# Performance work log

Hardware: AMD Instinct MI355X
Metric: run time of the kernel (lower is better)

The kernel has to match this reference:

```python
import jax, jax.numpy as jnp
import numpy as np

B, T, D = 32, 1024, 1024
PCA_DIM = 256
NS = 4
NC = 1024
SEC = PCA_DIM // NS


def setup_inputs() -> dict:
    key = jax.random.key(0)
    k1, k2, k3 = jax.random.split(key, 3)
    inputs = jax.random.normal(k1, (B, T, D), dtype=jnp.float32)
    # variance_scaling(1.0, 'fan_avg', 'normal'): std = sqrt(2 / (fan_in + fan_out))
    pca_proj = jax.random.normal(k2, (D, PCA_DIM), dtype=jnp.float32) * np.float32(np.sqrt(2.0 / (D + PCA_DIM)))
    pre_bias = jnp.zeros((1, D), dtype=jnp.float32)
    # per-section codebooks, variance_scaling(0.1, 'fan_avg', 'normal')
    codebooks = jax.random.normal(k3, (NS, NC, SEC), dtype=jnp.float32) * np.float32(np.sqrt(0.1 * 2.0 / (NC + SEC)))
    return {"inputs": inputs, "pca_proj": pca_proj, "pre_bias": pre_bias, "codebooks": codebooks}


def reference(inputs, pca_proj, pre_bias, codebooks):
    in_shape = inputs.shape
    d = in_shape[-1]
    flat = inputs.reshape(-1, d)  # [N, D]
    n = flat.shape[0]
    # --- PCA projection + reconstruction / decorrelation losses ---
    projected = (flat + pre_bias) @ pca_proj            # [N, P]
    unprojected = projected @ pca_proj.T - pre_bias     # [N, D]
    l2_loss = jnp.mean(jnp.sqrt(jnp.sum(jnp.square(flat - unprojected), axis=-1)))
    cov = projected.T @ projected / n                   # [P, P]
    cov_loss = jnp.mean(jnp.square(cov - jnp.eye(pca_proj.shape[1], dtype=projected.dtype)))
    pca_loss = l2_loss + cov_loss
    # --- per-section vector quantization ---
    ns, nc, sec = codebooks.shape
    secs = projected.reshape(n, ns, sec).transpose(1, 0, 2)  # [ns, N, sec] == jnp.split along -1

    def quantize_section(x, cb):
        # x: [N, sec], cb: [nc, sec]; squared-L2 cdist via expansion
        dist = (jnp.sum(x * x, axis=1, keepdims=True)
                - 2.0 * (x @ cb.T)
                + jnp.sum(cb * cb, axis=1)[None, :])    # [N, nc]
        idx = jnp.argmin(dist, axis=1)                  # [N]
        q = cb[idx]                                     # gather == one_hot @ cb
        loss = jnp.square(q - jax.lax.stop_gradient(x))  # [N, sec]
        q_st = x + jax.lax.stop_gradient(q - x)         # straight-through
        return q_st, loss, idx

    q, sec_loss, idx = jax.vmap(quantize_section)(secs, codebooks)  # [ns,N,sec] x2, [ns,N]
    quantized = q.transpose(1, 0, 2).reshape(n, ns * sec)           # concat sections -> [N, P]
    quantized = (quantized @ pca_proj.T - pre_bias).reshape(in_shape)  # pca_unproject
    nn_idx = idx.reshape((ns,) + in_shape[:-1])                     # [ns, B, T]
    quantization_loss = jnp.mean(sec_loss.reshape((ns,) + in_shape[:-1] + (sec,)), axis=0) + pca_loss
    codebook = jax.lax.stop_gradient(codebooks.reshape(ns * nc, sec))
    cluster_counts = jnp.ones((ns, nc), dtype=jnp.float32)  # eval mode: jnp.ones init, no EMA
    return quantized, quantization_loss, nn_idx, codebook, cluster_counts
```

## Files before the change

kernel.cpp:

```cpp
#include <hip/hip_runtime.h>
#include <math.h>

#define NROW 32768
#define DIM  1024
#define PDIM 256
#define NSEC 4
#define NCODE 1024
#define SECD 64

__global__ __launch_bounds__(256, 4) void k_proj(const float* __restrict__ X,
                                                 const float* __restrict__ W,
                                                 const float* __restrict__ bias,
                                                 float* __restrict__ p0) {
    __shared__ __align__(16) float As[16][68];
    __shared__ __align__(16) float Bs[16][256];
    const int t  = threadIdx.x;
    const int ry = t >> 5;
    const int rx = t & 31;
    const int rb = blockIdx.x * 64;
    const int z  = blockIdx.z;
    const int k0 = z * 384;
    const int kn = (z == 2) ? 256 : 384;
    const int lr = t >> 2;
    const int ks = (t & 3) * 4;
    const int wv = t >> 6;
    const int ln = t & 63;
    const int gsw = ((ln & 31) << 1) | (ln >> 5);
    float* outp = p0 + (size_t)z * ((size_t)NROW * PDIM);
    float acc[8][8] = {};
    for (int kc = k0; kc < k0 + kn; kc += 16) {
        #pragma unroll
        for (int j = 0; j < 4; ++j) {
            const int krow = wv * 4 + j;
            __builtin_amdgcn_global_load_lds(
                (const __attribute__((address_space(1))) void*)(W + (size_t)(kc + krow) * PDIM + gsw * 4),
                (__attribute__((address_space(3))) void*)(&Bs[krow][0]),
                16, 0, 0);
        }
        float4 a = *(const float4*)&X[(size_t)(rb + lr) * DIM + kc + ks];
        float4 c = *(const float4*)&bias[kc + ks];
        As[ks + 0][lr] = a.x + c.x;
        As[ks + 1][lr] = a.y + c.y;
        As[ks + 2][lr] = a.z + c.z;
        As[ks + 3][lr] = a.w + c.w;
        __syncthreads();
        #pragma unroll
        for (int k = 0; k < 16; ++k) {
            float4 x0 = *(const float4*)&As[k][ry * 8];
            float4 x1 = *(const float4*)&As[k][ry * 8 + 4];
            float4 y0 = *(const float4*)&Bs[k][rx * 4];
            float4 y1 = *(const float4*)&Bs[k][128 + rx * 4];
            float aa[8] = {x0.x, x0.y, x0.z, x0.w, x1.x, x1.y, x1.z, x1.w};
            float bb[8] = {y0.x, y0.y, y0.z, y0.w, y1.x, y1.y, y1.z, y1.w};
            #pragma unroll
            for (int i = 0; i < 8; ++i)
                #pragma unroll
                for (int j = 0; j < 8; ++j)
                    acc[i][j] = fmaf(aa[i], bb[j], acc[i][j]);
        }
        __syncthreads();
    }
    #pragma unroll
    for (int i = 0; i < 8; ++i) {
        const size_t base = (size_t)(rb + ry * 8 + i) * PDIM + rx * 8;
        *(float4*)&outp[base]     = make_float4(acc[i][0], acc[i][1], acc[i][2], acc[i][3]);
        *(float4*)&outp[base + 4] = make_float4(acc[i][4], acc[i][5], acc[i][6], acc[i][7]);
    }
}

__global__ __launch_bounds__(256) void k_comb(float* __restrict__ p) {
    const size_t i = ((size_t)blockIdx.x * 256 + threadIdx.x) * 4;
    float4 a = *(const float4*)&p[i];
    float4 b = *(const float4*)&p[i + 8388608];
    float4 c = *(const float4*)&p[i + 16777216];
    float4 r;
    r.x = __fadd_rn(__fadd_rn(a.x, b.x), c.x);
    r.y = __fadd_rn(__fadd_rn(a.y, b.y), c.y);
    r.z = __fadd_rn(__fadd_rn(a.z, b.z), c.z);
    r.w = __fadd_rn(__fadd_rn(a.w, b.w), c.w);
    *(float4*)&p[i] = r;
}

__global__ __launch_bounds__(256, 4) void k_pm(const float* __restrict__ P,
                                               const float* __restrict__ M,
                                               float* __restrict__ PMa,
                                               float* __restrict__ PMb) {
    __shared__ __align__(16) float As[16][68];
    __shared__ __align__(16) float Bs[16][256];
    const int t  = threadIdx.x;
    const int ry = t >> 5;
    const int rx = t & 31;
    const int rb = blockIdx.x * 64;
    const int z  = blockIdx.z;
    const int k0 = z * 128;
    const int lr = t >> 2;
    const int ks = (t & 3) * 4;
    const int wv = t >> 6;
    const int ln = t & 63;
    const int gsw = ((ln & 31) << 1) | (ln >> 5);
    float* outp = z ? PMb : PMa;
    float acc[8][8] = {};
    for (int kc = k0; kc < k0 + 128; kc += 16) {
        #pragma unroll
        for (int j = 0; j < 4; ++j) {
            const int krow = wv * 4 + j;
            __builtin_amdgcn_global_load_lds(
                (const __attribute__((address_space(1))) void*)(M + (size_t)(kc + krow) * PDIM + gsw * 4),
                (__attribute__((address_space(3))) void*)(&Bs[krow][0]),
                16, 0, 0);
        }
        float4 a = *(const float4*)&P[(size_t)(rb + lr) * PDIM + kc + ks];
        As[ks + 0][lr] = a.x;
        As[ks + 1][lr] = a.y;
        As[ks + 2][lr] = a.z;
        As[ks + 3][lr] = a.w;
        __syncthreads();
        #pragma unroll
        for (int k = 0; k < 16; ++k) {
            float4 x0 = *(const float4*)&As[k][ry * 8];
            float4 x1 = *(const float4*)&As[k][ry * 8 + 4];
            float4 y0 = *(const float4*)&Bs[k][rx * 4];
            float4 y1 = *(const float4*)&Bs[k][128 + rx * 4];
            float aa[8] = {x0.x, x0.y, x0.z, x0.w, x1.x, x1.y, x1.z, x1.w};
            float bb[8] = {y0.x, y0.y, y0.z, y0.w, y1.x, y1.y, y1.z, y1.w};
            #pragma unroll
            for (int i = 0; i < 8; ++i)
                #pragma unroll
                for (int j = 0; j < 8; ++j)
                    acc[i][j] = fmaf(aa[i], bb[j], acc[i][j]);
        }
        __syncthreads();
    }
    #pragma unroll
    for (int i = 0; i < 8; ++i) {
        const size_t base = (size_t)(rb + ry * 8 + i) * PDIM + rx * 8;
        *(float4*)&outp[base]     = make_float4(acc[i][0], acc[i][1], acc[i][2], acc[i][3]);
        *(float4*)&outp[base + 4] = make_float4(acc[i][4], acc[i][5], acc[i][6], acc[i][7]);
    }
}

__global__ __launch_bounds__(256) void k_wtw(const float* __restrict__ W,
                                             float* __restrict__ M) {
    __shared__ float As[16][64];
    __shared__ float Bs[16][64];
    const int t = threadIdx.x;
    const int tx = t & 15, ty = t >> 4;
    const int ib = blockIdx.x * 64;
    const int jb = blockIdx.y * 64;
    const int sk = t >> 4;
    const int sc = (t & 15) * 4;
    float acc[4][4] = {};
    for (int kc = 0; kc < DIM; kc += 16) {
        float4 a = *(const float4*)&W[(size_t)(kc + sk) * PDIM + ib + sc];
        float4 b = *(const float4*)&W[(size_t)(kc + sk) * PDIM + jb + sc];
        *(float4*)&As[sk][sc] = a;
        *(float4*)&Bs[sk][sc] = b;
        __syncthreads();
        #pragma unroll
        for (int k = 0; k < 16; ++k) {
            float4 a4 = *(const float4*)&As[k][ty * 4];
            float4 b4 = *(const float4*)&Bs[k][tx * 4];
            float aa[4] = {a4.x, a4.y, a4.z, a4.w};
            float bb[4] = {b4.x, b4.y, b4.z, b4.w};
            #pragma unroll
            for (int i = 0; i < 4; ++i)
                #pragma unroll
                for (int j = 0; j < 4; ++j)
                    acc[i][j] = fmaf(aa[i], bb[j], acc[i][j]);
        }
        __syncthreads();
    }
    #pragma unroll
    for (int i = 0; i < 4; ++i)
        #pragma unroll
        for (int j = 0; j < 4; ++j)
            M[(size_t)(ib + ty * 4 + i) * PDIM + jb + tx * 4 + j] = acc[i][j];
}

__global__ __launch_bounds__(256) void k_xn2(const float* __restrict__ X,
                                             const float* __restrict__ bias,
                                             float* __restrict__ xn2) {
    const int n = blockIdx.x * 4 + (threadIdx.x >> 6);
    const int lane = threadIdx.x & 63;
    float s = 0.0f;
    #pragma unroll
    for (int i = 0; i < 4; ++i) {
        float4 x = *(const float4*)&X[(size_t)n * DIM + i * 256 + lane * 4];
        float4 b = *(const float4*)&bias[i * 256 + lane * 4];
        float vx = x.x + b.x, vy = x.y + b.y, vz = x.z + b.z, vw = x.w + b.w;
        s = fmaf(vx, vx, s); s = fmaf(vy, vy, s);
        s = fmaf(vz, vz, s); s = fmaf(vw, vw, s);
    }
    #pragma unroll
    for (int o = 1; o < 64; o <<= 1) s += __shfl_xor(s, o);
    if (lane == 0) xn2[n] = s;
}

__global__ __launch_bounds__(256) void k_rowres(const float* __restrict__ P,
                                                const float* __restrict__ PMa,
                                                const float* __restrict__ PMb,
                                                const float* __restrict__ xn2,
                                                float* __restrict__ rowres) {
    const int n = blockIdx.x * 4 + (threadIdx.x >> 6);
    const int lane = threadIdx.x & 63;
    float4 p  = *(const float4*)&P[(size_t)n * PDIM + lane * 4];
    float4 pa = *(const float4*)&PMa[(size_t)n * PDIM + lane * 4];
    float4 pb = *(const float4*)&PMb[(size_t)n * PDIM + lane * 4];
    float s = 0.0f;
    s = fmaf(p.x, (pa.x + pb.x) - 2.0f * p.x, s);
    s = fmaf(p.y, (pa.y + pb.y) - 2.0f * p.y, s);
    s = fmaf(p.z, (pa.z + pb.z) - 2.0f * p.z, s);
    s = fmaf(p.w, (pa.w + pb.w) - 2.0f * p.w, s);
    #pragma unroll
    for (int o = 1; o < 64; o <<= 1) s += __shfl_xor(s, o);
    if (lane == 0) rowres[n] = xn2[n] + s;
}

__global__ __launch_bounds__(256) void k_cov(const float* __restrict__ Pm,
                                             float* __restrict__ cov) {
    __shared__ float As[16][64];
    __shared__ float Bs[16][64];
    const int t = threadIdx.x;
    const int tx = t & 15, ty = t >> 4;
    const int ib = blockIdx.x * 64;
    const int jb = blockIdx.y * 64;
    const int nb = blockIdx.z * 512;
    const int sk = t >> 4;
    const int sc = (t & 15) * 4;
    float acc[4][4] = {};
    for (int kc = 0; kc < 512; kc += 16) {
        float4 a = *(const float4*)&Pm[(size_t)(nb + kc + sk) * PDIM + ib + sc];
        float4 b = *(const float4*)&Pm[(size_t)(nb + kc + sk) * PDIM + jb + sc];
        *(float4*)&As[sk][sc] = a;
        *(float4*)&Bs[sk][sc] = b;
        __syncthreads();
        #pragma unroll
        for (int k = 0; k < 16; ++k) {
            float4 a4 = *(const float4*)&As[k][ty * 4];
            float4 b4 = *(const float4*)&Bs[k][tx * 4];
            float aa[4] = {a4.x, a4.y, a4.z, a4.w};
            float bb[4] = {b4.x, b4.y, b4.z, b4.w};
            #pragma unroll
            for (int i = 0; i < 4; ++i)
                #pragma unroll
                for (int j = 0; j < 4; ++j)
                    acc[i][j] = fmaf(aa[i], bb[j], acc[i][j]);
        }
        __syncthreads();
    }
    #pragma unroll
    for (int i = 0; i < 4; ++i)
        #pragma unroll
        for (int j = 0; j < 4; ++j)
            atomicAdd(&cov[(size_t)(ib + ty * 4 + i) * PDIM + jb + tx * 4 + j], acc[i][j]);
}

__global__ __launch_bounds__(256) void k_covloss(const float* __restrict__ cov,
                                                 float* __restrict__ scal) {
    const int t = threadIdx.x;
    float s = 0.0f;
    for (int e = t; e < PDIM * PDIM; e += 256) {
        int i = e >> 8, j = e & 255;
        float v = cov[e] * (1.0f / 32768.0f) - (i == j ? 1.0f : 0.0f);
        s = fmaf(v, v, s);
    }
    #pragma unroll
    for (int o = 1; o < 64; o <<= 1) s += __shfl_xor(s, o);
    __shared__ float r4[4];
    if ((t & 63) == 0) r4[t >> 6] = s;
    __syncthreads();
    if (t == 0) scal[1] = (r4[0] + r4[1] + r4[2] + r4[3]) * (1.0f / 65536.0f);
}

__global__ __launch_bounds__(256) void k_l2(const float* __restrict__ rowres,
                                            float* __restrict__ scal) {
    int r = blockIdx.x * 256 + threadIdx.x;
    float v = sqrtf(rowres[r]);
    #pragma unroll
    for (int o = 1; o < 64; o <<= 1) v += __shfl_xor(v, o);
    if ((threadIdx.x & 63) == 0) atomicAdd(&scal[0], v);
}

__global__ __launch_bounds__(256) void k_cnorm(const float* __restrict__ cbs,
                                               float* __restrict__ cnorm) {
    int c = blockIdx.x * 256 + threadIdx.x;
    const float* p = &cbs[(size_t)c * SECD];
    float a[8];
    #pragma unroll
    for (int j = 0; j < 8; ++j) a[j] = __fmul_rn(p[j], p[j]);
    #pragma unroll
    for (int i = 8; i < 64; i += 8)
        #pragma unroll
        for (int j = 0; j < 8; ++j)
            a[j] = __fadd_rn(a[j], __fmul_rn(p[i + j], p[i + j]));
    float r = __fadd_rn(__fadd_rn(__fadd_rn(a[0], a[1]), __fadd_rn(a[2], a[3])),
                        __fadd_rn(__fadd_rn(a[4], a[5]), __fadd_rn(a[6], a[7])));
    cnorm[c] = r;
}

__global__ __launch_bounds__(256) void k_vq(const float* __restrict__ proj,
                                            const float* __restrict__ cbs,
                                            const float* __restrict__ cnorm,
                                            int* __restrict__ widx,
                                            float* __restrict__ out_idx,
                                            float* __restrict__ qpart) {
    __shared__ float xs[64][64];
    __shared__ float cs[64][128];
    __shared__ float xnorm[64];
    __shared__ int   sidx[64];
    const int t = threadIdx.x;
    const int ry = t >> 5;
    const int tx = t & 31;
    const int rb = blockIdx.x * 64;
    const int s  = blockIdx.y;
    const int lr = t >> 2;
    const int kq = (t & 3) * 16;
    const int cr = t >> 1;
    const int ko = (t & 1) * 32;

    #pragma unroll
    for (int i = 0; i < 16; i += 4) {
        float4 v = *(const float4*)&proj[(size_t)(rb + lr) * PDIM + s * SECD + kq + i];
        xs[kq + i + 0][lr] = v.x; xs[kq + i + 1][lr] = v.y;
        xs[kq + i + 2][lr] = v.z; xs[kq + i + 3][lr] = v.w;
    }
    __syncthreads();
    if (t < 64) {
        float a[8];
        #pragma unroll
        for (int j = 0; j < 8; ++j) { float v = xs[j][t]; a[j] = __fmul_rn(v, v); }
        #pragma unroll
        for (int i = 8; i < 64; i += 8)
            #pragma unroll
            for (int j = 0; j < 8; ++j) {
                float v = xs[i + j][t];
                a[j] = __fadd_rn(a[j], __fmul_rn(v, v));
            }
        xnorm[t] = __fadd_rn(__fadd_rn(__fadd_rn(a[0], a[1]), __fadd_rn(a[2], a[3])),
                             __fadd_rn(__fadd_rn(a[4], a[5]), __fadd_rn(a[6], a[7])));
    }
    float best[8]; int bidx[8];
    #pragma unroll
    for (int i = 0; i < 8; ++i) { best[i] = 3.4e38f; bidx[i] = 0; }

    for (int ct = 0; ct < 8; ++ct) {
        __syncthreads();
        #pragma unroll
        for (int u = 0; u < 32; u += 4) {
            float4 v = *(const float4*)&cbs[(size_t)(s * NCODE + ct * 128 + cr) * SECD + ko + u];
            cs[ko + u + 0][cr] = v.x; cs[ko + u + 1][cr] = v.y;
            cs[ko + u + 2][cr] = v.z; cs[ko + u + 3][cr] = v.w;
        }
        __syncthreads();
        float4 cn4 = *(const float4*)&cnorm[s * NCODE + ct * 128 + tx * 4];
        float cna[4] = {cn4.x, cn4.y, cn4.z, cn4.w};
        float acc[8][4] = {};
        #pragma unroll 8
        for (int k = 0; k < 64; ++k) {
            float4 x0 = *(const float4*)&xs[k][ry * 8];
            float4 x1 = *(const float4*)&xs[k][ry * 8 + 4];
            float4 b4 = *(const float4*)&cs[k][tx * 4];
            float aa[8] = {x0.x, x0.y, x0.z, x0.w, x1.x, x1.y, x1.z, x1.w};
            float bb[4] = {b4.x, b4.y, b4.z, b4.w};
            #pragma unroll
            for (int i = 0; i < 8; ++i)
                #pragma unroll
                for (int j = 0; j < 4; ++j)
                    acc[i][j] = fmaf(aa[i], bb[j], acc[i][j]);
        }
        #pragma unroll
        for (int i = 0; i < 8; ++i) {
            float xn = xnorm[ry * 8 + i];
            #pragma unroll
            for (int j = 0; j < 4; ++j) {
                float d = __fadd_rn(__fsub_rn(xn, __fmul_rn(2.0f, acc[i][j])), cna[j]);
                int code = ct * 128 + tx * 4 + j;
                if (d < best[i]) { best[i] = d; bidx[i] = code; }
            }
        }
    }
    #pragma unroll
    for (int i = 0; i < 8; ++i) {
        float d = best[i]; int ix = bidx[i];
        #pragma unroll
        for (int o = 1; o < 32; o <<= 1) {
            float od = __shfl_xor(d, o);
            int   oi = __shfl_xor(ix, o);
            if (od < d || (od == d && oi < ix)) { d = od; ix = oi; }
        }
        if (tx == 0) {
            int row = rb + ry * 8 + i;
            widx[s * NROW + row] = ix;
            out_idx[s * NROW + row] = (float)ix;
            sidx[ry * 8 + i] = ix;
        }
    }
    __syncthreads();
    {
        const float* crow = &cbs[(size_t)(s * NCODE + sidx[lr]) * SECD];
        #pragma unroll
        for (int i = 0; i < 16; i += 4) {
            float4 q = *(const float4*)&crow[kq + i];
            float qq[4] = {q.x, q.y, q.z, q.w};
            float r[4];
            #pragma unroll
            for (int u = 0; u < 4; ++u) {
                float d = qq[u] - xs[kq + i + u][lr];
                r[u] = __fmul_rn(d, d);
            }
            *(float4*)&qpart[((size_t)s * NROW + rb + lr) * SECD + kq + i] =
                make_float4(r[0], r[1], r[2], r[3]);
        }
    }
}

__global__ __launch_bounds__(256) void k_cbu(const float* __restrict__ cbs,
                                             const float* __restrict__ W,
                                             float* __restrict__ cbu) {
    __shared__ float As[16][64];
    __shared__ float Bs[16][64];
    const int t = threadIdx.x;
    const int tx = t & 15, ty = t >> 4;
    const int s = blockIdx.z;
    const int cbase = blockIdx.y * 64;
    const int db = blockIdx.x * 64;
    const int lr = t >> 2;
    const int lk = (t & 3) * 4;
    float acc[4][4] = {};
    for (int kc = 0; kc < SECD; kc += 16) {
        float4 a = *(const float4*)&cbs[(size_t)(s * NCODE + cbase + lr) * SECD + kc + lk];
        float4 b = *(const float4*)&W[(size_t)(db + lr) * PDIM + s * SECD + kc + lk];
        As[lk + 0][lr] = a.x; As[lk + 1][lr] = a.y;
        As[lk + 2][lr] = a.z; As[lk + 3][lr] = a.w;
        Bs[lk + 0][lr] = b.x; Bs[lk + 1][lr] = b.y;
        Bs[lk + 2][lr] = b.z; Bs[lk + 3][lr] = b.w;
        __syncthreads();
        #pragma unroll
        for (int k = 0; k < 16; ++k) {
            float4 a4 = *(const float4*)&As[k][ty * 4];
            float4 b4 = *(const float4*)&Bs[k][tx * 4];
            float aa[4] = {a4.x, a4.y, a4.z, a4.w};
            float bb[4] = {b4.x, b4.y, b4.z, b4.w};
            #pragma unroll
            for (int i = 0; i < 4; ++i)
                #pragma unroll
                for (int j = 0; j < 4; ++j)
                    acc[i][j] = fmaf(aa[i], bb[j], acc[i][j]);
        }
        __syncthreads();
    }
    #pragma unroll
    for (int i = 0; i < 4; ++i) {
        float4 v = make_float4(acc[i][0], acc[i][1], acc[i][2], acc[i][3]);
        *(float4*)&cbu[(size_t)(s * NCODE + cbase + ty * 4 + i) * DIM + db + tx * 4] = v;
    }
}

__global__ __launch_bounds__(256) void k_gather(const float* __restrict__ cbu,
                                                const int* __restrict__ widx,
                                                const float* __restrict__ bias,
                                                float* __restrict__ out0) {
    const int n = blockIdx.x;
    const int d = threadIdx.x * 4;
    int i0 = widx[0 * NROW + n];
    int i1 = widx[1 * NROW + n];
    int i2 = widx[2 * NROW + n];
    int i3 = widx[3 * NROW + n];
    float4 v0 = *(const float4*)&cbu[((size_t)(0 * NCODE + i0)) * DIM + d];
    float4 v1 = *(const float4*)&cbu[((size_t)(1 * NCODE + i1)) * DIM + d];
    float4 v2 = *(const float4*)&cbu[((size_t)(2 * NCODE + i2)) * DIM + d];
    float4 v3 = *(const float4*)&cbu[((size_t)(3 * NCODE + i3)) * DIM + d];
    float4 b = *(const float4*)&bias[d];
    float4 r;
    r.x = v0.x + v1.x + v2.x + v3.x - b.x;
    r.y = v0.y + v1.y + v2.y + v3.y - b.y;
    r.z = v0.z + v1.z + v2.z + v3.z - b.z;
    r.w = v0.w + v1.w + v2.w + v3.w - b.w;
    *(float4*)&out0[(size_t)n * DIM + d] = r;
}

__global__ __launch_bounds__(256) void k_addpca(float* __restrict__ out1,
                                                const float* __restrict__ qpart,
                                                const float* __restrict__ scal) {
    float pca = scal[0] * (1.0f / 32768.0f) + scal[1];
    const size_t e = ((size_t)blockIdx.x * 256 + threadIdx.x) * 4;
    float4 a = *(const float4*)&qpart[e];
    float4 b = *(const float4*)&qpart[e + 2097152];
    float4 c = *(const float4*)&qpart[e + 4194304];
    float4 d = *(const float4*)&qpart[e + 6291456];
    float4 r;
    r.x = 0.25f * __fadd_rn(__fadd_rn(__fadd_rn(a.x, b.x), c.x), d.x) + pca;
    r.y = 0.25f * __fadd_rn(__fadd_rn(__fadd_rn(a.y, b.y), c.y), d.y) + pca;
    r.z = 0.25f * __fadd_rn(__fadd_rn(__fadd_rn(a.z, b.z), c.z), d.z) + pca;
    r.w = 0.25f * __fadd_rn(__fadd_rn(__fadd_rn(a.w, b.w), c.w), d.w) + pca;
    *(float4*)&out1[e] = r;
}

__global__ __launch_bounds__(256) void k_tail(const float* __restrict__ cbs,
                                              float* __restrict__ out3,
                                              float* __restrict__ out4) {
    int e = blockIdx.x * 256 + threadIdx.x;
    ((float4*)out3)[e] = ((const float4*)cbs)[e];
    if (e < 4096) out4[e] = 1.0f;
}

extern "C" void kernel_launch(void* const* d_in, const int* in_sizes, int n_in,
                              void* d_out, int out_size, void* d_ws, size_t ws_size,
                              hipStream_t stream) {
    (void)in_sizes; (void)n_in; (void)out_size; (void)ws_size;
    const float* X    = (const float*)d_in[0];
    const float* W    = (const float*)d_in[1];
    const float* bias = (const float*)d_in[2];
    const float* cbs  = (const float*)d_in[3];

    float* out  = (float*)d_out;
    float* out0 = out;
    float* out1 = out + 33554432;
    float* out2 = out + 35651584;
    float* out3 = out + 35782656;
    float* out4 = out + 36044800;

    char* ws = (char*)d_ws;
    float* cbu    = (float*)(ws);
    float* rowres = (float*)(ws + 16777216);
    float* cov    = (float*)(ws + 16908288);
    float* scal   = (float*)(ws + 17170432);
    float* cnorm  = (float*)(ws + 17170496);
    int*   widx   = (int*)  (ws + 17186880);
    float* wtw    = (float*)(ws + 17711168);

    float* proj  = out0;
    float* PMa   = out0 + 8388608;
    float* PMb   = out0 + 25165824;
    float* qpart = out0 + 8388608;
    float* xn2  = out1;

    hipMemsetAsync(ws + 16908288, 0, 262144 + 64, stream);

    k_proj    <<<dim3(512, 1, 3), 256, 0, stream>>>(X, W, bias, proj);
    k_comb    <<<8192,            256, 0, stream>>>(proj);
    k_xn2     <<<8192,            256, 0, stream>>>(X, bias, xn2);
    k_wtw     <<<dim3(4, 4),      256, 0, stream>>>(W, wtw);
    k_cov     <<<dim3(4, 4, 64),  256, 0, stream>>>(proj, cov);
    k_covloss <<<1,               256, 0, stream>>>(cov, scal);
    k_pm      <<<dim3(512, 1, 2), 256, 0, stream>>>(proj, wtw, PMa, PMb);
    k_rowres  <<<8192,            256, 0, stream>>>(proj, PMa, PMb, xn2, rowres);
    k_l2      <<<128,             256, 0, stream>>>(rowres, scal);
    k_cnorm   <<<16,              256, 0, stream>>>(cbs, cnorm);
    k_vq      <<<dim3(512, 4),    256, 0, stream>>>(proj, cbs, cnorm, widx, out2, qpart);
    k_cbu     <<<dim3(16, 16, 4), 256, 0, stream>>>(cbs, W, cbu);
    k_gather  <<<32768,           256, 0, stream>>>(cbu, widx, bias, out0);
    k_addpca  <<<2048,            256, 0, stream>>>(out1, qpart, scal);
    k_tail    <<<256,             256, 0, stream>>>(cbs, out3, out4);
}
```

Before: 1.057 ms.

## Restructure VQ kernel to keep one row per thread in registers

```diff
diff --git a/kernel.cpp b/kernel.cpp
--- a/kernel.cpp
+++ b/kernel.cpp
@@ -298,118 +298,105 @@
     cnorm[c] = r;
 }
 
-__global__ __launch_bounds__(256) void k_vq(const float* __restrict__ proj,
-                                            const float* __restrict__ cbs,
-                                            const float* __restrict__ cnorm,
-                                            int* __restrict__ widx,
-                                            float* __restrict__ out_idx,
-                                            float* __restrict__ qpart) {
-    __shared__ float xs[64][64];
-    __shared__ float cs[64][128];
-    __shared__ float xnorm[64];
-    __shared__ int   sidx[64];
-    const int t = threadIdx.x;
-    const int ry = t >> 5;
-    const int tx = t & 31;
+__global__ __launch_bounds__(256, 3) void k_vq(const float* __restrict__ proj,
+                                               const float* __restrict__ cbs,
+                                               const float* __restrict__ cnorm,
+                                               int* __restrict__ widx,
+                                               float* __restrict__ out_idx,
+                                               float* __restrict__ qpart) {
+    __shared__ __align__(16) float xs[64][68];
+    __shared__ __align__(16) float cs[128][64];
+    __shared__ float wbest[4][64];
+    __shared__ int   wbidx[4][64];
+    const int t  = threadIdx.x;
+    const int wv = t >> 6;
+    const int ln = t & 63;
     const int rb = blockIdx.x * 64;
     const int s  = blockIdx.y;
-    const int lr = t >> 2;
-    const int kq = (t & 3) * 16;
-    const int cr = t >> 1;
-    const int ko = (t & 1) * 32;
-
-    #pragma unroll
-    for (int i = 0; i < 16; i += 4) {
-        float4 v = *(const float4*)&proj[(size_t)(rb + lr) * PDIM + s * SECD + kq + i];
-        xs[kq + i + 0][lr] = v.x; xs[kq + i + 1][lr] = v.y;
-        xs[kq + i + 2][lr] = v.z; xs[kq + i + 3][lr] = v.w;
+    const int row = rb + ln;
+
+    {
+        const int r = t >> 2, kb = (t & 3) * 16;
+        #pragma unroll
+        for (int u = 0; u < 16; u += 4) {
+            float4 v = *(const float4*)&proj[(size_t)(rb + r) * PDIM + s * SECD + kb + u];
+            *(float4*)&xs[r][kb + u] = v;
+        }
     }
     __syncthreads();
-    if (t < 64) {
-        float a[8];
-        #pragma unroll
-        for (int j = 0; j < 8; ++j) { float v = xs[j][t]; a[j] = __fmul_rn(v, v); }
-        #pragma unroll
-        for (int i = 8; i < 64; i += 8)
+    float x[64];
+    #pragma unroll
+    for (int i = 0; i < 64; i += 4) {
+        float4 v = *(const float4*)&xs[ln][i];
+        x[i] = v.x; x[i + 1] = v.y; x[i + 2] = v.z; x[i + 3] = v.w;
+    }
+    float a8[8];
+    #pragma unroll
+    for (int j = 0; j < 8; ++j) a8[j] = __fmul_rn(x[j], x[j]);
+    #pragma unroll
+    for (int i = 8; i < 64; i += 8)
+        #pragma unroll
+        for (int j = 0; j < 8; ++j)
+            a8[j] = __fadd_rn(a8[j], __fmul_rn(x[i + j], x[i + j]));
+    const float xn = __fadd_rn(__fadd_rn(__fadd_rn(a8[0], a8[1]), __fadd_rn(a8[2], a8[3])),
+                               __fadd_rn(__fadd_rn(a8[4], a8[5]), __fadd_rn(a8[6], a8[7])));
+
+    float best = 3.4e38f; int bcode = 0;
+    for (int ct = 0; ct < 8; ++ct) {
+        __syncthreads();
+        {
+            const int cr = t >> 1, ko = (t & 1) * 32;
+            #pragma unroll
+            for (int u = 0; u < 32; u += 4) {
+                float4 v = *(const float4*)&cbs[(size_t)(s * NCODE + ct * 128 + cr) * SECD + ko + u];
+                *(float4*)&cs[cr][ko + u] = v;
+            }
+        }
+        __syncthreads();
+        #pragma unroll 1
+        for (int cb = 0; cb < 32; cb += 8) {
+            const int c0 = wv * 32 + cb;
+            float acc[8] = {};
+            #pragma unroll
+            for (int kk = 0; kk < 64; kk += 4) {
+                #pragma unroll
+                for (int j = 0; j < 8; ++j) {
+                    float4 c4 = *(const float4*)&cs[c0 + j][kk];
+                    acc[j] = fmaf(x[kk],     c4.x, acc[j]);
+                    acc[j] = fmaf(x[kk + 1], c4.y, acc[j]);
+                    acc[j] = fmaf(x[kk + 2], c4.z, acc[j]);
+                    acc[j] = fmaf(x[kk + 3], c4.w, acc[j]);
+                }
+            }
             #pragma unroll
             for (int j = 0; j < 8; ++j) {
-                float v = xs[i + j][t];
-                a[j] = __fadd_rn(a[j], __fmul_rn(v, v));
+                const int code = ct * 128 + c0 + j;
+                float d = __fadd_rn(__fsub_rn(xn, __fmul_rn(2.0f, acc[j])),
+                                    cnorm[s * NCODE + code]);
+                if (d < best) { best = d; bcode = code; }
             }
-        xnorm[t] = __fadd_rn(__fadd_rn(__fadd_rn(a[0], a[1]), __fadd_rn(a[2], a[3])),
-                             __fadd_rn(__fadd_rn(a[4], a[5]), __fadd_rn(a[6], a[7])));
-    }
-    float best[8]; int bidx[8];
-    #pragma unroll
-    for (int i = 0; i < 8; ++i) { best[i] = 3.4e38f; bidx[i] = 0; }
-
-    for (int ct = 0; ct < 8; ++ct) {
-        __syncthreads();
-        #pragma unroll
-        for (int u = 0; u < 32; u += 4) {
-            float4 v = *(const float4*)&cbs[(size_t)(s * NCODE + ct * 128 + cr) * SECD + ko + u];
-            cs[ko + u + 0][cr] = v.x; cs[ko + u + 1][cr] = v.y;
-            cs[ko + u + 2][cr] = v.z; cs[ko + u + 3][cr] = v.w;
-        }
-        __syncthreads();
-        float4 cn4 = *(const float4*)&cnorm[s * NCODE + ct * 128 + tx * 4];
-        float cna[4] = {cn4.x, cn4.y, cn4.z, cn4.w};
-        float acc[8][4] = {};
-        #pragma unroll 8
-        for (int k = 0; k < 64; ++k) {
-            float4 x0 = *(const float4*)&xs[k][ry * 8];
-            float4 x1 = *(const float4*)&xs[k][ry * 8 + 4];
-            float4 b4 = *(const float4*)&cs[k][tx * 4];
-            float aa[8] = {x0.x, x0.y, x0.z, x0.w, x1.x, x1.y, x1.z, x1.w};
-            float bb[4] = {b4.x, b4.y, b4.z, b4.w};
-            #pragma unroll
-            for (int i = 0; i < 8; ++i)
-                #pragma unroll
-                for (int j = 0; j < 4; ++j)
-                    acc[i][j] = fmaf(aa[i], bb[j], acc[i][j]);
-        }
-        #pragma unroll
-        for (int i = 0; i < 8; ++i) {
-            float xn = xnorm[ry * 8 + i];
-            #pragma unroll
-            for (int j = 0; j < 4; ++j) {
-                float d = __fadd_rn(__fsub_rn(xn, __fmul_rn(2.0f, acc[i][j])), cna[j]);
-                int code = ct * 128 + tx * 4 + j;
-                if (d < best[i]) { best[i] = d; bidx[i] = code; }
-            }
-        }
-    }
-    #pragma unroll
-    for (int i = 0; i < 8; ++i) {
-        float d = best[i]; int ix = bidx[i];
-        #pragma unroll
-        for (int o = 1; o < 32; o <<= 1) {
-            float od = __shfl_xor(d, o);
-            int   oi = __shfl_xor(ix, o);
+        }
+    }
+    wbest[wv][ln] = best; wbidx[wv][ln] = bcode;
+    __syncthreads();
+    if (wv == 0) {
+        float d = wbest[0][ln]; int ix = wbidx[0][ln];
+        #pragma unroll
+        for (int w = 1; w < 4; ++w) {
+            float od = wbest[w][ln]; int oi = wbidx[w][ln];
             if (od < d || (od == d && oi < ix)) { d = od; ix = oi; }
         }
-        if (tx == 0) {
-            int row = rb + ry * 8 + i;
-            widx[s * NROW + row] = ix;
-            out_idx[s * NROW + row] = (float)ix;
-            sidx[ry * 8 + i] = ix;
-        }
-    }
-    __syncthreads();
-    {
-        const float* crow = &cbs[(size_t)(s * NCODE + sidx[lr]) * SECD];
-        #pragma unroll
-        for (int i = 0; i < 16; i += 4) {
-            float4 q = *(const float4*)&crow[kq + i];
-            float qq[4] = {q.x, q.y, q.z, q.w};
-            float r[4];
-            #pragma unroll
-            for (int u = 0; u < 4; ++u) {
-                float d = qq[u] - xs[kq + i + u][lr];
-                r[u] = __fmul_rn(d, d);
-            }
-            *(float4*)&qpart[((size_t)s * NROW + rb + lr) * SECD + kq + i] =
-                make_float4(r[0], r[1], r[2], r[3]);
+        widx[s * NROW + row] = ix;
+        out_idx[s * NROW + row] = (float)ix;
+        const float* crow = &cbs[(size_t)(s * NCODE + ix) * SECD];
+        #pragma unroll
+        for (int i = 0; i < 64; i += 4) {
+            float4 q = *(const float4*)&crow[i];
+            float d0 = q.x - x[i],     d1 = q.y - x[i + 1];
+            float d2 = q.z - x[i + 2], d3 = q.w - x[i + 3];
+            *(float4*)&qpart[((size_t)s * NROW + row) * SECD + i] =
+                make_float4(__fmul_rn(d0, d0), __fmul_rn(d1, d1),
+                            __fmul_rn(d2, d2), __fmul_rn(d3, d3));
         }
     }
 }
@@ -548,8 +535,8 @@
     k_l2      <<<128,             256, 0, stream>>>(rowres, scal);
     k_cnorm   <<<16,              256, 0, stream>>>(cbs, cnorm);
     k_vq      <<<dim3(512, 4),    256, 0, stream>>>(proj, cbs, cnorm, widx, out2, qpart);
+    k_addpca  <<<2048,            256, 0, stream>>>(out1, qpart, scal);
     k_cbu     <<<dim3(16, 16, 4), 256, 0, stream>>>(cbs, W, cbu);
     k_gather  <<<32768,           256, 0, stream>>>(cbu, widx, bias, out0);
-    k_addpca  <<<2048,            256, 0, stream>>>(out1, qpart, scal);
     k_tail    <<<256,             256, 0, stream>>>(cbs, out3, out4);
 }
```

Measured after the change: 1.313 ms. 24.2% more time.
